# Optimization experiments

Measured on AMD Instinct MI355X. Metric: run time of the kernel, lower is better.

The kernel has to match this reference:

```python
import jax, jax.numpy as jnp
import numpy as np

DIM = 128
N_GNN = 3
B, N1, N2 = 8, 128, 512
VDW_N = 6.0
DEV_VDW = 0.2
MAX_VDW, MIN_VDW = 0.0356, 0.0178
DM_MIN = 0.5


def setup_inputs() -> dict:
    key = jax.random.key(0)
    ks = jax.random.split(key, 24)
    f32 = jnp.float32
    h1 = jax.random.normal(ks[0], (B, N1, 54), f32)
    h2 = jax.random.normal(ks[1], (B, N2, 54), f32)
    a1 = (jax.random.uniform(ks[2], (B, N1, N1)) < 0.1).astype(f32)
    adj1 = jnp.clip(a1 + jnp.swapaxes(a1, 1, 2) + jnp.eye(N1, dtype=f32), 0.0, 1.0)
    a2 = (jax.random.uniform(ks[3], (B, N2, N2)) < 0.05).astype(f32)
    adj2 = jnp.clip(a2 + jnp.swapaxes(a2, 1, 2) + jnp.eye(N2, dtype=f32), 0.0, 1.0)
    A_int = (jax.random.uniform(ks[4], (B, 8, N1, N2)) < 0.05).astype(f32)
    pos1 = jax.random.uniform(ks[5], (B, N1, 3), f32) * 30.0
    pos2 = jax.random.uniform(ks[6], (B, N2, 3), f32) * 30.0
    rotor = jax.random.uniform(ks[7], (B,), f32) * 10.0
    vdw_radius1 = 1.0 + jax.random.uniform(ks[8], (B, N1), f32)
    vdw_radius2 = 1.0 + jax.random.uniform(ks[9], (B, N2), f32)
    delta_uff = jax.random.uniform(ks[10], (B,), f32)
    no_metal1 = jnp.ones((B, N1), f32)
    no_metal2 = jnp.ones((B, N2), f32)
    s = 0.1
    node_W = jax.random.normal(ks[11], (54, DIM), f32) * s
    gat_W = jax.random.normal(ks[12], (N_GNN, DIM, DIM), f32) * s
    gat_b = jnp.zeros((N_GNN, DIM), f32)
    gat_A = jax.random.normal(ks[13], (N_GNN, DIM, DIM), f32) * s
    gate_W = jax.random.normal(ks[14], (N_GNN, 2 * DIM), f32) * s
    gate_b = jnp.zeros((N_GNN,), f32)
    vdwA_W1 = jax.random.normal(ks[15], (2 * DIM, 128), f32) * s
    vdwA_b1 = jnp.zeros((128,), f32)
    vdwA_W2 = jax.random.normal(ks[16], (128,), f32) * s
    vdwA_b2 = jnp.zeros((1,), f32)
    vdwB_W1 = jax.random.normal(ks[17], (2 * DIM, 128), f32) * s
    vdwB_b1 = jnp.zeros((128,), f32)
    vdwB_W2 = jax.random.normal(ks[18], (128,), f32) * s
    vdwB_b2 = jnp.zeros((1,), f32)
    hbond_coeff = jnp.array([1.0], f32)
    hydrophobic_coeff = jnp.array([0.5], f32)
    vdw_coeff = jnp.array([1.0], f32)
    rotor_coeff = jnp.array([0.5], f32)
    return dict(h1=h1, adj1=adj1, h2=h2, adj2=adj2, A_int=A_int, pos1=pos1, pos2=pos2,
                rotor=rotor, vdw_radius1=vdw_radius1, vdw_radius2=vdw_radius2,
                delta_uff=delta_uff, no_metal1=no_metal1, no_metal2=no_metal2,
                node_W=node_W, gat_W=gat_W, gat_b=gat_b, gat_A=gat_A, gate_W=gate_W,
                gate_b=gate_b, vdwA_W1=vdwA_W1, vdwA_b1=vdwA_b1, vdwA_W2=vdwA_W2,
                vdwA_b2=vdwA_b2, vdwB_W1=vdwB_W1, vdwB_b1=vdwB_b1, vdwB_W2=vdwB_W2,
                vdwB_b2=vdwB_b2, hbond_coeff=hbond_coeff,
                hydrophobic_coeff=hydrophobic_coeff, vdw_coeff=vdw_coeff,
                rotor_coeff=rotor_coeff)


def _gat(x, adj, W, b, A, gW, gb):
    # PIGNet GAT_gate: attention softmax over axis=1, masked by adj, gated residual.
    h = x @ W + b                                   # [B,N,D]
    e = jnp.einsum('bil,bkl->bik', h @ A, h)        # [B,N,N]
    e = e + jnp.swapaxes(e, 1, 2)
    att = jnp.where(adj > 0, e, -9e15)
    att = jax.nn.softmax(att, axis=1) * adj
    h_prime = jax.nn.relu(jnp.einsum('bij,bjk->bik', att, h))
    coeff = jax.nn.sigmoid(jnp.concatenate([x, h_prime], -1) @ gW + gb)[..., None]
    return coeff * x + (1.0 - coeff) * h_prime


def _pair_mlp(g1, g2, W1, b1, w2, b2):
    # Equivalent to Linear(cat[h1_rep,h2_rep]) without materializing the 2D concat.
    z = (jnp.einsum('bik,kh->bih', g1, W1[:DIM])[:, :, None, :]
         + jnp.einsum('bjk,kh->bjh', g2, W1[DIM:])[:, None, :, :] + b1)  # [B,N1,N2,128]
    return jax.nn.relu(z) @ w2 + b2                 # [B,N1,N2]


def _forward(h1, adj1, h2, adj2, A_int, pos1, pos2, rotor, vdw_radius1, vdw_radius2,
             delta_uff, no_metal1, no_metal2, node_W, gat_W, gat_b, gat_A, gate_W,
             gate_b, vdwA_W1, vdwA_b1, vdwA_W2, vdwA_b2, vdwB_W1, vdwB_b1, vdwB_W2,
             vdwB_b2, hbond_coeff, hydrophobic_coeff, vdw_coeff, rotor_coeff):
    g1 = h1 @ node_W
    g2 = h2 @ node_W
    for i in range(N_GNN):
        g1 = _gat(g1, adj1, gat_W[i], gat_b[i], gat_A[i], gate_W[i], gate_b[i])
        g2 = _gat(g2, adj2, gat_W[i], gat_b[i], gat_A[i], gate_W[i], gate_b[i])
    diff = pos1[:, :, None, :] - pos2[:, None, :, :]
    dm = jnp.sqrt(jnp.sum(diff * diff, -1) + 1e-10)   # [B,N1,N2]
    dm = jnp.where(dm < DM_MIN, 1e10, dm)
    A_w = jax.nn.sigmoid(_pair_mlp(g1, g2, vdwA_W1, vdwA_b1, vdwA_W2, vdwA_b2))
    B_w = jnp.tanh(_pair_mlp(g1, g2, vdwB_W1, vdwB_b1, vdwB_W2, vdwB_b2)) * DEV_VDW
    dm0 = vdw_radius1[:, :, None] + vdw_radius2[:, None, :] + B_w
    # vdW 12-6 term
    dm0_safe = jnp.where(dm0 < 1e-4, 1.0, dm0)
    rN = (dm0_safe / dm) ** VDW_N
    evdw = jnp.minimum(rN * rN - 2.0 * rN, 100.0)
    mask12 = no_metal1[:, :, None] * no_metal2[:, None, :]
    Aamp = A_w * (MAX_VDW - MIN_VDW) + MIN_VDW
    E_vdw = jnp.sum(Aamp * evdw * mask12, axis=(1, 2))
    # hbond / hydrophobic terms use unfixed dm0
    dmd = dm - dm0
    hb = -(hbond_coeff * hbond_coeff)[0]
    hy = -(hydrophobic_coeff * hydrophobic_coeff)[0]
    E_hb1 = jnp.sum(jnp.clip(dmd * A_int[:, 1] / -0.7, 0.0, 1.0), axis=(1, 2)) * hb
    E_hb2 = jnp.sum(jnp.clip(dmd * A_int[:, -1] / -0.7, 0.0, 1.0), axis=(1, 2)) * hb
    E_hp = jnp.sum(jnp.clip((-dmd + 1.5) * A_int[:, -2], 0.0, 1.0), axis=(1, 2)) * hy
    E_t = delta_uff * (vdw_coeff * vdw_coeff)[0]
    ret = jnp.stack([E_vdw, E_hb1, E_hb2, E_hp, E_t], -1)   # [B,5]
    ret = ret / (1.0 + (rotor_coeff * rotor_coeff)[0] * rotor[:, None])
    return ret


def reference(h1, adj1, h2, adj2, A_int, pos1, pos2, rotor, vdw_radius1, vdw_radius2,
              delta_uff, no_metal1, no_metal2, node_W, gat_W, gat_b, gat_A, gate_W,
              gate_b, vdwA_W1, vdwA_b1, vdwA_W2, vdwA_b2, vdwB_W1, vdwB_b1, vdwB_W2,
              vdwB_b2, hbond_coeff, hydrophobic_coeff, vdw_coeff, rotor_coeff):
    return _forward(h1, adj1, h2, adj2, A_int, pos1, pos2, rotor, vdw_radius1,
                    vdw_radius2, delta_uff, no_metal1, no_metal2, node_W, gat_W,
                    gat_b, gat_A, gate_W, gate_b, vdwA_W1, vdwA_b1, vdwA_W2,
                    vdwA_b2, vdwB_W1, vdwB_b1, vdwB_W2, vdwB_b2, hbond_coeff,
                    hydrophobic_coeff, vdw_coeff, rotor_coeff)
```

## Files before the change

### kernel.cpp

```cpp
#include <hip/hip_runtime.h>
#include <math.h>

#define D 128
#define NB 8
#define NN1 128
#define NN2 512
#define ROWS1 (NB * NN1)
#define ROWS2 (NB * NN2)
#define ROWS (ROWS1 + ROWS2)
#define CAP1 96
#define CAP2 160
#define CSR_ELEMS ((size_t)ROWS1 * CAP1 + (size_t)ROWS2 * CAP2)

__device__ __forceinline__ void resolve_row(int row, int& base_row, size_t& cbase,
                                            int& N) {
    if (row < ROWS1) {
        base_row = row & ~127;
        cbase = (size_t)row * CAP1;
        N = NN1;
    } else {
        int r = row - ROWS1;
        base_row = ROWS1 + (r & ~511);
        cbase = (size_t)ROWS1 * CAP1 + (size_t)r * CAP2;
        N = NN2;
    }
}

__global__ __launch_bounds__(128) void k_csrembed(
    const float* __restrict__ h1, const float* __restrict__ h2,
    const float* __restrict__ adj1, const float* __restrict__ adj2,
    const float* __restrict__ W, float* __restrict__ g,
    unsigned short* __restrict__ csr, int* __restrict__ nnz,
    float* __restrict__ out) {
    int row = blockIdx.x;
    int t = threadIdx.x;
    if (row == 0 && t < NB * 5) out[t] = 0.f;
    const float* src = (row < ROWS1) ? h1 + (size_t)row * 54
                                     : h2 + (size_t)(row - ROWS1) * 54;
    __shared__ float xr[56];
    if (t < 54) xr[t] = src[t];
    __syncthreads();
    float a0 = 0.f, a1 = 0.f;
#pragma unroll
    for (int k = 0; k < 54; k += 2) {
        a0 += xr[k] * W[k * D + t];
        if (k + 1 < 54) a1 += xr[k + 1] * W[(k + 1) * D + t];
    }
    g[(size_t)row * D + t] = a0 + a1;

    if (t < 64) {
        int base_row, N;
        size_t cbase;
        resolve_row(row, base_row, cbase, N);
        int cap = (row < ROWS1) ? CAP1 : CAP2;
        const float* arow = (row < ROWS1)
                                ? adj1 + (size_t)row * NN1
                                : adj2 + (size_t)(row - ROWS1) * NN2;
        int cnt = 0;
        for (int c0 = 0; c0 < N; c0 += 64) {
            float v = arow[c0 + t];
            unsigned long long m = __ballot(v > 0.f);
            int rank = __popcll(m & ((1ull << t) - 1ull));
            if (v > 0.f && cnt + rank < cap)
                csr[cbase + cnt + rank] = (unsigned short)(c0 + t);
            cnt += __popcll(m);
        }
        if (t == 0) nnz[row] = cnt < cap ? cnt : cap;
    }
}

__global__ __launch_bounds__(256) void k_h(const float* __restrict__ g,
                                           const float* __restrict__ W,
                                           const float* __restrict__ bias,
                                           const float* __restrict__ A,
                                           float* __restrict__ h, float* __restrict__ hA) {
    int row0 = blockIdx.x * 16;
    int t = threadIdx.x;
    int d = t & 127, rh = t >> 7;
    __shared__ float xs[16][D];
    __shared__ float hs[16][D];
    {
        int r = t >> 4, c = (t & 15) * 8;
        *(float4*)&xs[r][c] = *(const float4*)&g[((size_t)row0 + r) * D + c];
        *(float4*)&xs[r][c + 4] = *(const float4*)&g[((size_t)row0 + r) * D + c + 4];
    }
    __syncthreads();
    float bv = bias[d];
    float acc[8];
#pragma unroll
    for (int u = 0; u < 8; ++u) acc[u] = bv;
    for (int k0 = 0; k0 < D; k0 += 4) {
        float w0 = W[(k0 + 0) * D + d];
        float w1 = W[(k0 + 1) * D + d];
        float w2 = W[(k0 + 2) * D + d];
        float w3 = W[(k0 + 3) * D + d];
#pragma unroll
        for (int u = 0; u < 8; ++u) {
            float4 xv = *(const float4*)&xs[rh * 8 + u][k0];
            acc[u] += xv.x * w0 + xv.y * w1 + xv.z * w2 + xv.w * w3;
        }
    }
#pragma unroll
    for (int u = 0; u < 8; ++u) {
        int r = rh * 8 + u;
        h[((size_t)row0 + r) * D + d] = acc[u];
        hs[r][d] = acc[u];
    }
    __syncthreads();
    float acc2[8];
#pragma unroll
    for (int u = 0; u < 8; ++u) acc2[u] = 0.f;
    for (int k0 = 0; k0 < D; k0 += 4) {
        float w0 = A[(k0 + 0) * D + d];
        float w1 = A[(k0 + 1) * D + d];
        float w2 = A[(k0 + 2) * D + d];
        float w3 = A[(k0 + 3) * D + d];
#pragma unroll
        for (int u = 0; u < 8; ++u) {
            float4 xv = *(const float4*)&hs[rh * 8 + u][k0];
            acc2[u] += xv.x * w0 + xv.y * w1 + xv.z * w2 + xv.w * w3;
        }
    }
#pragma unroll
    for (int u = 0; u < 8; ++u)
        hA[((size_t)row0 + rh * 8 + u) * D + d] = acc2[u];
}

__global__ __launch_bounds__(128) void k_Ssp(const float* __restrict__ h,
                                             const float* __restrict__ hA,
                                             const unsigned short* __restrict__ csr,
                                             const int* __restrict__ nnz,
                                             float* __restrict__ svals,
                                             float2* __restrict__ rowstat) {
    int row = blockIdx.x;
    int t = threadIdx.x;
    int base_row, N;
    size_t cbase;
    resolve_row(row, base_row, cbase, N);
    int n = nnz[row];
    int grp = t >> 4, u = t & 15;
    const float* hrow = h + (size_t)row * D + u * 8;
    const float* hArow = hA + (size_t)row * D + u * 8;
    float4 hi0 = *(const float4*)&hrow[0], hi1 = *(const float4*)&hrow[4];
    float4 ai0 = *(const float4*)&hArow[0], ai1 = *(const float4*)&hArow[4];
    __shared__ float sv[CAP2];
    for (int s0 = 0; s0 < n; s0 += 16) {
        int sa = s0 + grp;
        int sb = sa + 8;
        float pa = 0.f, pb = 0.f;
        if (sa < n) {
            int jrow = base_row + csr[cbase + sa];
            const float* hj = h + (size_t)jrow * D + u * 8;
            const float* aj = hA + (size_t)jrow * D + u * 8;
            float4 hj0 = *(const float4*)&hj[0], hj1 = *(const float4*)&hj[4];
            float4 aj0 = *(const float4*)&aj[0], aj1 = *(const float4*)&aj[4];
            pa = hi0.x * aj0.x + hi0.y * aj0.y + hi0.z * aj0.z + hi0.w * aj0.w +
                 hi1.x * aj1.x + hi1.y * aj1.y + hi1.z * aj1.z + hi1.w * aj1.w +
                 ai0.x * hj0.x + ai0.y * hj0.y + ai0.z * hj0.z + ai0.w * hj0.w +
                 ai1.x * hj1.x + ai1.y * hj1.y + ai1.z * hj1.z + ai1.w * hj1.w;
        }
        if (sb < n) {
            int jrow = base_row + csr[cbase + sb];
            const float* hj = h + (size_t)jrow * D + u * 8;
            const float* aj = hA + (size_t)jrow * D + u * 8;
            float4 hj0 = *(const float4*)&hj[0], hj1 = *(const float4*)&hj[4];
            float4 aj0 = *(const float4*)&aj[0], aj1 = *(const float4*)&aj[4];
            pb = hi0.x * aj0.x + hi0.y * aj0.y + hi0.z * aj0.z + hi0.w * aj0.w +
                 hi1.x * aj1.x + hi1.y * aj1.y + hi1.z * aj1.z + hi1.w * aj1.w +
                 ai0.x * hj0.x + ai0.y * hj0.y + ai0.z * hj0.z + ai0.w * hj0.w +
                 ai1.x * hj1.x + ai1.y * hj1.y + ai1.z * hj1.z + ai1.w * hj1.w;
        }
#pragma unroll
        for (int o = 8; o > 0; o >>= 1) {
            pa += __shfl_xor(pa, o);
            pb += __shfl_xor(pb, o);
        }
        if (u == 0) {
            if (sa < n) sv[sa] = pa;
            if (sb < n) sv[sb] = pb;
        }
    }
    __syncthreads();
    if (t < 64) {
        float m = -3.4e38f;
        for (int s = t; s < n; s += 64) m = fmaxf(m, sv[s]);
#pragma unroll
        for (int o = 32; o > 0; o >>= 1) m = fmaxf(m, __shfl_xor(m, o));
        float sum = 0.f;
        for (int s = t; s < n; s += 64) sum += expf(sv[s] - m);
#pragma unroll
        for (int o = 32; o > 0; o >>= 1) sum += __shfl_xor(sum, o);
        if (t == 0) rowstat[row] = make_float2(m, 1.f / sum);
    }
    for (int s = t; s < n; s += 128) svals[cbase + s] = sv[s];
}

__global__ __launch_bounds__(128) void k_hpgate(const float* __restrict__ hbuf,
                                                float* __restrict__ g,
                                                const float* __restrict__ svals,
                                                const float2* __restrict__ rowstat,
                                                const unsigned short* __restrict__ csr,
                                                const int* __restrict__ nnz,
                                                const float* __restrict__ gW,
                                                const float* __restrict__ gb) {
    int row = blockIdx.x;
    int d = threadIdx.x;
    int base_row, N;
    size_t cbase;
    resolve_row(row, base_row, cbase, N);
    int n = nnz[row];
    __shared__ float avals[CAP2];
    __shared__ int aidx[CAP2];
    __shared__ float red[128];
    for (int s = d; s < n; s += 128) {
        int jrow = base_row + csr[cbase + s];
        float2 st = rowstat[jrow];
        avals[s] = expf(svals[cbase + s] - st.x) * st.y;
        aidx[s] = jrow;
    }
    __syncthreads();
    float a[8];
#pragma unroll
    for (int u = 0; u < 8; ++u) a[u] = 0.f;
    int s = 0;
    for (; s + 8 <= n; s += 8) {
#pragma unroll
        for (int u = 0; u < 8; ++u)
            a[u] += avals[s + u] * hbuf[(size_t)aidx[s + u] * D + d];
    }
    for (; s < n; ++s) a[0] += avals[s] * hbuf[(size_t)aidx[s] * D + d];
    float hv = fmaxf(((a[0] + a[1]) + (a[2] + a[3])) + ((a[4] + a[5]) + (a[6] + a[7])),
                     0.f);
    float xv = g[(size_t)row * D + d];
    red[d] = xv * gW[d] + hv * gW[D + d];
    __syncthreads();
    for (int o = 64; o > 0; o >>= 1) {
        if (d < o) red[d] += red[d + o];
        __syncthreads();
    }
    float c = 1.f / (1.f + expf(-(red[0] + gb[0])));
    g[(size_t)row * D + d] = c * xv + (1.f - c) * hv;
}

__global__ __launch_bounds__(256) void k_pairpre(const float* __restrict__ g,
                                                 const float* __restrict__ WA,
                                                 const float* __restrict__ WB,
                                                 const float* __restrict__ bA,
                                                 const float* __restrict__ bB,
                                                 float* __restrict__ aA,
                                                 float* __restrict__ aB) {
    int row0 = blockIdx.x * 16;
    int t = threadIdx.x;
    int d = t & 127, rh = t >> 7;
    int g2 = (row0 >= ROWS1);
    const float* WAp = g2 ? WA + D * D : WA;
    const float* WBp = g2 ? WB + D * D : WB;
    __shared__ float xs[16][D];
    {
        int r = t >> 4, c = (t & 15) * 8;
        *(float4*)&xs[r][c] = *(const float4*)&g[((size_t)row0 + r) * D + c];
        *(float4*)&xs[r][c + 4] = *(const float4*)&g[((size_t)row0 + r) * D + c + 4];
    }
    __syncthreads();
    float bvA = g2 ? 0.f : bA[d];
    float bvB = g2 ? 0.f : bB[d];
    float accA[8], accB[8];
#pragma unroll
    for (int u = 0; u < 8; ++u) { accA[u] = bvA; accB[u] = bvB; }
    for (int k0 = 0; k0 < D; k0 += 4) {
        float wa0 = WAp[(k0 + 0) * D + d], wa1 = WAp[(k0 + 1) * D + d];
        float wa2 = WAp[(k0 + 2) * D + d], wa3 = WAp[(k0 + 3) * D + d];
        float wb0 = WBp[(k0 + 0) * D + d], wb1 = WBp[(k0 + 1) * D + d];
        float wb2 = WBp[(k0 + 2) * D + d], wb3 = WBp[(k0 + 3) * D + d];
#pragma unroll
        for (int u = 0; u < 8; ++u) {
            float4 xv = *(const float4*)&xs[rh * 8 + u][k0];
            accA[u] += xv.x * wa0 + xv.y * wa1 + xv.z * wa2 + xv.w * wa3;
            accB[u] += xv.x * wb0 + xv.y * wb1 + xv.z * wb2 + xv.w * wb3;
        }
    }
#pragma unroll
    for (int u = 0; u < 8; ++u) {
        int r = rh * 8 + u;
        aA[((size_t)row0 + r) * D + d] = accA[u];
        aB[((size_t)row0 + r) * D + d] = accB[u];
    }
}

__global__ __launch_bounds__(256) void k_pairz(
    const float* __restrict__ aA, const float* __restrict__ aB,
    const float* __restrict__ w2A, const float* __restrict__ w2B,
    const float* __restrict__ b2A, const float* __restrict__ b2B,
    const float* __restrict__ pos1, const float* __restrict__ pos2,
    const float* __restrict__ vr1, const float* __restrict__ vr2,
    const float* __restrict__ nm1, const float* __restrict__ nm2,
    const float* __restrict__ A_int, const float* __restrict__ rotor,
    const float* __restrict__ duff, const float* __restrict__ hbond,
    const float* __restrict__ hydro, const float* __restrict__ vdwc,
    const float* __restrict__ rotc, float* __restrict__ out) {
    int b = blockIdx.y;
    int itile = blockIdx.x >> 4, jtile = blockIdx.x & 15;
    int i0 = itile * 32, j0 = jtile * 32;
    int t = threadIdx.x;
    int tx = t & 15, ty = t >> 4;
    __shared__ float A1a[32][20], A1b[32][20], A2a[32][20], A2b[32][20];
    __shared__ float w2As[128], w2Bs[128];
    __shared__ float zAs[32][33], zBs[32][33];
    __shared__ float redc[8][4];
    if (t < 128) { w2As[t] = w2A[t]; w2Bs[t] = w2B[t]; }
    float zA[2][2] = {{0.f, 0.f}, {0.f, 0.f}};
    float zB[2][2] = {{0.f, 0.f}, {0.f, 0.f}};
    int half = t >> 7, idx = t & 127;
    int sr = idx >> 2, sc = (idx & 3) * 4;
    size_t grow = half ? (size_t)(ROWS1 + b * NN2 + j0 + sr)
                       : (size_t)(b * NN1 + i0 + sr);
    for (int hc = 0; hc < D; hc += 16) {
        __syncthreads();
        float4 va = *(const float4*)&aA[grow * D + hc + sc];
        float4 vb = *(const float4*)&aB[grow * D + hc + sc];
        if (half) { *(float4*)&A2a[sr][sc] = va; *(float4*)&A2b[sr][sc] = vb; }
        else      { *(float4*)&A1a[sr][sc] = va; *(float4*)&A1b[sr][sc] = vb; }
        __syncthreads();
#pragma unroll
        for (int hh = 0; hh < 16; hh += 4) {
            float4 wA = *(const float4*)&w2As[hc + hh];
            float4 wB = *(const float4*)&w2Bs[hc + hh];
            float4 xA0 = *(const float4*)&A1a[ty][hh];
            float4 xA1 = *(const float4*)&A1a[ty + 16][hh];
            float4 xB0 = *(const float4*)&A1b[ty][hh];
            float4 xB1 = *(const float4*)&A1b[ty + 16][hh];
            float4 yA0 = *(const float4*)&A2a[tx][hh];
            float4 yA1 = *(const float4*)&A2a[tx + 16][hh];
            float4 yB0 = *(const float4*)&A2b[tx][hh];
            float4 yB1 = *(const float4*)&A2b[tx + 16][hh];
#define RD4(xx, yy, ww) (fmaxf(xx.x + yy.x, 0.f) * ww.x + fmaxf(xx.y + yy.y, 0.f) * ww.y + \
                         fmaxf(xx.z + yy.z, 0.f) * ww.z + fmaxf(xx.w + yy.w, 0.f) * ww.w)
            zA[0][0] += RD4(xA0, yA0, wA); zA[0][1] += RD4(xA0, yA1, wA);
            zA[1][0] += RD4(xA1, yA0, wA); zA[1][1] += RD4(xA1, yA1, wA);
            zB[0][0] += RD4(xB0, yB0, wB); zB[0][1] += RD4(xB0, yB1, wB);
            zB[1][0] += RD4(xB1, yB0, wB); zB[1][1] += RD4(xB1, yB1, wB);
#undef RD4
        }
    }
#pragma unroll
    for (int u = 0; u < 2; ++u)
#pragma unroll
        for (int v = 0; v < 2; ++v) {
            zAs[ty + 16 * u][tx + 16 * v] = zA[u][v];
            zBs[ty + 16 * u][tx + 16 * v] = zB[u][v];
        }
    __syncthreads();
    int j2 = t & 31, ig = t >> 5;
    int jg = j0 + j2;
    size_t j_off = (size_t)b * NN2 + jg;
    float p2x = pos2[j_off * 3 + 0], p2y = pos2[j_off * 3 + 1], p2z = pos2[j_off * 3 + 2];
    float r2 = vr2[j_off], m2 = nm2[j_off];
    float zb2A = b2A[0], zb2B = b2B[0];
    float eV[4], e1[4], e2[4], eH[4];
#pragma unroll
    for (int ii = 0; ii < 4; ++ii) {
        int il = ig * 4 + ii;
        int iglob = i0 + il;
        size_t i_off = (size_t)b * NN1 + iglob;
        float zAv = zAs[il][j2] + zb2A;
        float zBv = zBs[il][j2] + zb2B;
        float dx = pos1[i_off * 3 + 0] - p2x;
        float dy = pos1[i_off * 3 + 1] - p2y;
        float dz = pos1[i_off * 3 + 2] - p2z;
        float dm = sqrtf(dx * dx + dy * dy + dz * dz + 1e-10f);
        if (dm < 0.5f) dm = 1e10f;
        float A_w = 1.f / (1.f + expf(-zAv));
        float B_w = tanhf(zBv) * 0.2f;
        float dm0 = vr1[i_off] + r2 + B_w;
        float dm0s = (dm0 < 1e-4f) ? 1.f : dm0;
        float rr = dm0s / dm;
        float rr2 = rr * rr;
        float rN = rr2 * rr2 * rr2;
        float evdw = fminf(rN * rN - 2.f * rN, 100.f);
        float mask = nm1[i_off] * m2;
        float Aamp = A_w * (0.0356f - 0.0178f) + 0.0178f;
        eV[ii] = Aamp * evdw * mask;
        float dmd = dm - dm0;
        size_t abase = (((size_t)b * 8) * NN1 + iglob) * NN2 + jg;
        float Ai1 = A_int[abase + (size_t)1 * NN1 * NN2];
        float Ai6 = A_int[abase + (size_t)6 * NN1 * NN2];
        float Ai7 = A_int[abase + (size_t)7 * NN1 * NN2];
        e1[ii] = fminf(fmaxf(dmd * Ai1 * (-1.f / 0.7f), 0.f), 1.f);
        e2[ii] = fminf(fmaxf(dmd * Ai7 * (-1.f / 0.7f), 0.f), 1.f);
        eH[ii] = fminf(fmaxf((1.5f - dmd) * Ai6, 0.f), 1.f);
    }
    float sV = (eV[0] + eV[1]) + (eV[2] + eV[3]);
    float s1 = (e1[0] + e1[1]) + (e1[2] + e1[3]);
    float s2 = (e2[0] + e2[1]) + (e2[2] + e2[3]);
    float sH = (eH[0] + eH[1]) + (eH[2] + eH[3]);
#pragma unroll
    for (int o = 16; o > 0; o >>= 1) {
        sV += __shfl_xor(sV, o);
        s1 += __shfl_xor(s1, o);
        s2 += __shfl_xor(s2, o);
        sH += __shfl_xor(sH, o);
    }
    if (j2 == 0) {
        redc[ig][0] = sV; redc[ig][1] = s1; redc[ig][2] = s2; redc[ig][3] = sH;
    }
    __syncthreads();
    if (t < 4) {
        float v = 0.f;
#pragma unroll
        for (int gg = 0; gg < 8; ++gg) v += redc[gg][t];
        float scl = 1.f / (1.f + rotc[0] * rotc[0] * rotor[b]);
        float coef;
        if (t == 0) coef = scl;
        else if (t == 3) coef = -hydro[0] * hydro[0] * scl;
        else coef = -hbond[0] * hbond[0] * scl;
        atomicAdd(&out[b * 5 + t], v * coef);
    }
    if (t == 4 && itile == 0 && jtile == 0) {
        float scl = 1.f / (1.f + rotc[0] * rotc[0] * rotor[b]);
        atomicAdd(&out[b * 5 + 4], duff[b] * vdwc[0] * vdwc[0] * scl);
    }
}

extern "C" void kernel_launch(void* const* d_in, const int* in_sizes, int n_in,
                              void* d_out, int out_size, void* d_ws, size_t ws_size,
                              hipStream_t stream) {
    const float* h1    = (const float*)d_in[0];
    const float* adj1  = (const float*)d_in[1];
    const float* h2    = (const float*)d_in[2];
    const float* adj2  = (const float*)d_in[3];
    const float* A_int = (const float*)d_in[4];
    const float* pos1  = (const float*)d_in[5];
    const float* pos2  = (const float*)d_in[6];
    const float* rotor = (const float*)d_in[7];
    const float* vr1   = (const float*)d_in[8];
    const float* vr2   = (const float*)d_in[9];
    const float* duff  = (const float*)d_in[10];
    const float* nm1   = (const float*)d_in[11];
    const float* nm2   = (const float*)d_in[12];
    const float* nodeW = (const float*)d_in[13];
    const float* gatW  = (const float*)d_in[14];
    const float* gatb  = (const float*)d_in[15];
    const float* gatA  = (const float*)d_in[16];
    const float* gateW = (const float*)d_in[17];
    const float* gateb = (const float*)d_in[18];
    const float* vA_W1 = (const float*)d_in[19];
    const float* vA_b1 = (const float*)d_in[20];
    const float* vA_W2 = (const float*)d_in[21];
    const float* vA_b2 = (const float*)d_in[22];
    const float* vB_W1 = (const float*)d_in[23];
    const float* vB_b1 = (const float*)d_in[24];
    const float* vB_W2 = (const float*)d_in[25];
    const float* vB_b2 = (const float*)d_in[26];
    const float* hbond = (const float*)d_in[27];
    const float* hydro = (const float*)d_in[28];
    const float* vdwc  = (const float*)d_in[29];
    const float* rotc  = (const float*)d_in[30];

    float* p = (float*)d_ws;
    float* g     = p; p += (size_t)ROWS * D;
    float* hbuf  = p; p += (size_t)ROWS * D;
    float* hAbuf = p; p += (size_t)ROWS * D;
    float* svals = p; p += CSR_ELEMS;
    float2* rowstat = (float2*)p; p += 2 * (size_t)ROWS;
    unsigned short* csr = (unsigned short*)p;
    int* nnz = (int*)(csr + CSR_ELEMS);
    float* aA = hbuf;
    float* aB = hAbuf;

    k_csrembed<<<ROWS, 128, 0, stream>>>(h1, h2, adj1, adj2, nodeW, g, csr, nnz,
                                         (float*)d_out);

    for (int l = 0; l < 3; ++l) {
        const float* W  = gatW  + (size_t)l * D * D;
        const float* bb = gatb  + (size_t)l * D;
        const float* A  = gatA  + (size_t)l * D * D;
        const float* gW = gateW + (size_t)l * 2 * D;
        const float* gb = gateb + l;
        k_h<<<ROWS / 16, 256, 0, stream>>>(g, W, bb, A, hbuf, hAbuf);
        k_Ssp<<<ROWS, 128, 0, stream>>>(hbuf, hAbuf, csr, nnz, svals, rowstat);
        k_hpgate<<<ROWS, 128, 0, stream>>>(hbuf, g, svals, rowstat, csr, nnz, gW, gb);
    }

    k_pairpre<<<ROWS / 16, 256, 0, stream>>>(g, vA_W1, vB_W1, vA_b1, vB_b1, aA, aB);
    k_pairz<<<dim3(64, NB), 256, 0, stream>>>(aA, aB, vA_W2, vB_W2, vA_b2, vB_b2,
                                              pos1, pos2, vr1, vr2, nm1, nm2, A_int,
                                              rotor, duff, hbond, hydro, vdwc, rotc,
                                              (float*)d_out);
}
```

Measured before the change: 313.3 us.

## Fuse gated aggregation with next layer GEMMs and embed into first layer

Merges the per-row gate and aggregation kernel into the following layer's h/hA GEMM kernel, and the final layer's gate into the pair-pre GEMM. The node embedding is folded into the first h GEMM, and CSR construction moves to its own 4-rows-per-block kernel. Each 64-lane wave owns 4 rows, so no block barriers are needed, and the gate reduction uses wave shuffles. The h buffers are double-buffered so a layer can read neighbours while writing the next h. This cuts launches and global round trips of g. The cost is fewer blocks, with each wave processing its rows' gathers serially.

```diff
diff --git a/kernel.cpp b/kernel.cpp
--- a/kernel.cpp
+++ b/kernel.cpp
@@ -26,104 +26,105 @@
     }
 }
 
-__global__ __launch_bounds__(128) void k_csrembed(
-    const float* __restrict__ h1, const float* __restrict__ h2,
-    const float* __restrict__ adj1, const float* __restrict__ adj2,
-    const float* __restrict__ W, float* __restrict__ g,
-    unsigned short* __restrict__ csr, int* __restrict__ nnz,
-    float* __restrict__ out) {
-    int row = blockIdx.x;
+__global__ __launch_bounds__(256) void k_csr(const float* __restrict__ adj1,
+                                             const float* __restrict__ adj2,
+                                             unsigned short* __restrict__ csr,
+                                             int* __restrict__ nnz,
+                                             float* __restrict__ out) {
     int t = threadIdx.x;
-    if (row == 0 && t < NB * 5) out[t] = 0.f;
-    const float* src = (row < ROWS1) ? h1 + (size_t)row * 54
-                                     : h2 + (size_t)(row - ROWS1) * 54;
-    __shared__ float xr[56];
-    if (t < 54) xr[t] = src[t];
-    __syncthreads();
-    float a0 = 0.f, a1 = 0.f;
-#pragma unroll
-    for (int k = 0; k < 54; k += 2) {
-        a0 += xr[k] * W[k * D + t];
-        if (k + 1 < 54) a1 += xr[k + 1] * W[(k + 1) * D + t];
-    }
-    g[(size_t)row * D + t] = a0 + a1;
-
-    if (t < 64) {
-        int base_row, N;
-        size_t cbase;
-        resolve_row(row, base_row, cbase, N);
-        int cap = (row < ROWS1) ? CAP1 : CAP2;
-        const float* arow = (row < ROWS1)
-                                ? adj1 + (size_t)row * NN1
-                                : adj2 + (size_t)(row - ROWS1) * NN2;
-        int cnt = 0;
-        for (int c0 = 0; c0 < N; c0 += 64) {
-            float v = arow[c0 + t];
-            unsigned long long m = __ballot(v > 0.f);
-            int rank = __popcll(m & ((1ull << t) - 1ull));
-            if (v > 0.f && cnt + rank < cap)
-                csr[cbase + cnt + rank] = (unsigned short)(c0 + t);
-            cnt += __popcll(m);
-        }
-        if (t == 0) nnz[row] = cnt < cap ? cnt : cap;
-    }
-}
-
-__global__ __launch_bounds__(256) void k_h(const float* __restrict__ g,
-                                           const float* __restrict__ W,
-                                           const float* __restrict__ bias,
-                                           const float* __restrict__ A,
-                                           float* __restrict__ h, float* __restrict__ hA) {
+    if (blockIdx.x == 0 && t < NB * 5) out[t] = 0.f;
+    int row = blockIdx.x * 4 + (t >> 6);
+    int lane = t & 63;
+    int base_row, N;
+    size_t cbase;
+    resolve_row(row, base_row, cbase, N);
+    int cap = (row < ROWS1) ? CAP1 : CAP2;
+    const float* arow = (row < ROWS1) ? adj1 + (size_t)row * NN1
+                                      : adj2 + (size_t)(row - ROWS1) * NN2;
+    int cnt = 0;
+    for (int c0 = 0; c0 < N; c0 += 64) {
+        float v = arow[c0 + lane];
+        unsigned long long m = __ballot(v > 0.f);
+        int rank = __popcll(m & ((1ull << lane) - 1ull));
+        if (v > 0.f && cnt + rank < cap)
+            csr[cbase + cnt + rank] = (unsigned short)(c0 + lane);
+        cnt += __popcll(m);
+    }
+    if (lane == 0) nnz[row] = cnt < cap ? cnt : cap;
+}
+
+#define GEMM16(XS, W, B0, B1, OUTSTMT)                                        \
+    {                                                                         \
+        float acc[4][2];                                                      \
+        _Pragma("unroll") for (int u = 0; u < 4; ++u) {                       \
+            acc[u][0] = (B0); acc[u][1] = (B1);                               \
+        }                                                                     \
+        for (int k0 = 0; k0 < D; k0 += 4) {                                   \
+            float w00 = (W)[(k0 + 0) * D + d0], w01 = (W)[(k0 + 0) * D + d0 + 64]; \
+            float w10 = (W)[(k0 + 1) * D + d0], w11 = (W)[(k0 + 1) * D + d0 + 64]; \
+            float w20 = (W)[(k0 + 2) * D + d0], w21 = (W)[(k0 + 2) * D + d0 + 64]; \
+            float w30 = (W)[(k0 + 3) * D + d0], w31 = (W)[(k0 + 3) * D + d0 + 64]; \
+            _Pragma("unroll") for (int u = 0; u < 4; ++u) {                   \
+                float4 xv = *(const float4*)&XS[rg * 4 + u][k0];              \
+                acc[u][0] += xv.x * w00 + xv.y * w10 + xv.z * w20 + xv.w * w30; \
+                acc[u][1] += xv.x * w01 + xv.y * w11 + xv.z * w21 + xv.w * w31; \
+            }                                                                 \
+        }                                                                     \
+        _Pragma("unroll") for (int u = 0; u < 4; ++u) {                       \
+            _Pragma("unroll") for (int hf = 0; hf < 2; ++hf) {                \
+                int rr = rg * 4 + u;                                          \
+                int dd = d0 + hf * 64;                                        \
+                float av = acc[u][hf];                                        \
+                OUTSTMT;                                                      \
+            }                                                                 \
+        }                                                                     \
+    }
+
+__global__ __launch_bounds__(256) void k_h0(
+    const float* __restrict__ h1in, const float* __restrict__ h2in,
+    const float* __restrict__ nodeW, const float* __restrict__ W,
+    const float* __restrict__ bias, const float* __restrict__ A,
+    float* __restrict__ g, float* __restrict__ hOut, float* __restrict__ hAOut) {
     int row0 = blockIdx.x * 16;
     int t = threadIdx.x;
-    int d = t & 127, rh = t >> 7;
+    int d0 = t & 63, rg = t >> 6;
+    __shared__ float hin[16][56];
     __shared__ float xs[16][D];
     __shared__ float hs[16][D];
     {
-        int r = t >> 4, c = (t & 15) * 8;
-        *(float4*)&xs[r][c] = *(const float4*)&g[((size_t)row0 + r) * D + c];
-        *(float4*)&xs[r][c + 4] = *(const float4*)&g[((size_t)row0 + r) * D + c + 4];
-    }
-    __syncthreads();
-    float bv = bias[d];
-    float acc[8];
-#pragma unroll
-    for (int u = 0; u < 8; ++u) acc[u] = bv;
-    for (int k0 = 0; k0 < D; k0 += 4) {
-        float w0 = W[(k0 + 0) * D + d];
-        float w1 = W[(k0 + 1) * D + d];
-        float w2 = W[(k0 + 2) * D + d];
-        float w3 = W[(k0 + 3) * D + d];
-#pragma unroll
-        for (int u = 0; u < 8; ++u) {
-            float4 xv = *(const float4*)&xs[rh * 8 + u][k0];
-            acc[u] += xv.x * w0 + xv.y * w1 + xv.z * w2 + xv.w * w3;
-        }
-    }
-#pragma unroll
-    for (int u = 0; u < 8; ++u) {
-        int r = rh * 8 + u;
-        h[((size_t)row0 + r) * D + d] = acc[u];
-        hs[r][d] = acc[u];
-    }
-    __syncthreads();
-    float acc2[8];
-#pragma unroll
-    for (int u = 0; u < 8; ++u) acc2[u] = 0.f;
-    for (int k0 = 0; k0 < D; k0 += 4) {
-        float w0 = A[(k0 + 0) * D + d];
-        float w1 = A[(k0 + 1) * D + d];
-        float w2 = A[(k0 + 2) * D + d];
-        float w3 = A[(k0 + 3) * D + d];
-#pragma unroll
-        for (int u = 0; u < 8; ++u) {
-            float4 xv = *(const float4*)&hs[rh * 8 + u][k0];
-            acc2[u] += xv.x * w0 + xv.y * w1 + xv.z * w2 + xv.w * w3;
-        }
-    }
-#pragma unroll
-    for (int u = 0; u < 8; ++u)
-        hA[((size_t)row0 + rh * 8 + u) * D + d] = acc2[u];
+        int lane = t & 63;
+        const float* src = (row0 < ROWS1) ? h1in + (size_t)row0 * 54
+                                          : h2in + (size_t)(row0 - ROWS1) * 54;
+        for (int idx = lane; idx < 4 * 54; idx += 64) {
+            int r = idx / 54, c = idx - r * 54;
+            hin[rg * 4 + r][c] = src[(size_t)(rg * 4 + r) * 54 + c];
+        }
+    }
+    {
+        float acc[4][2] = {{0.f,0.f},{0.f,0.f},{0.f,0.f},{0.f,0.f}};
+        for (int k = 0; k < 54; ++k) {
+            float w0 = nodeW[k * D + d0], w1 = nodeW[k * D + d0 + 64];
+#pragma unroll
+            for (int u = 0; u < 4; ++u) {
+                float x = hin[rg * 4 + u][k];
+                acc[u][0] += x * w0;
+                acc[u][1] += x * w1;
+            }
+        }
+#pragma unroll
+        for (int u = 0; u < 4; ++u)
+#pragma unroll
+            for (int hf = 0; hf < 2; ++hf) {
+                int rr = rg * 4 + u, dd = d0 + hf * 64;
+                xs[rr][dd] = acc[u][hf];
+                g[((size_t)row0 + rr) * D + dd] = acc[u][hf];
+            }
+    }
+    float b0 = bias[d0], b1 = bias[d0 + 64];
+    GEMM16(xs, W, b0, b1,
+           { hs[rr][dd] = av; hOut[((size_t)row0 + rr) * D + dd] = av; })
+    GEMM16(hs, A, 0.f, 0.f,
+           { hAOut[((size_t)row0 + rr) * D + dd] = av; })
 }
 
 __global__ __launch_bounds__(128) void k_Ssp(const float* __restrict__ h,
@@ -195,96 +196,108 @@
     for (int s = t; s < n; s += 128) svals[cbase + s] = sv[s];
 }
 
-__global__ __launch_bounds__(128) void k_hpgate(const float* __restrict__ hbuf,
-                                                float* __restrict__ g,
-                                                const float* __restrict__ svals,
-                                                const float2* __restrict__ rowstat,
-                                                const unsigned short* __restrict__ csr,
-                                                const int* __restrict__ nnz,
-                                                const float* __restrict__ gW,
-                                                const float* __restrict__ gb) {
-    int row = blockIdx.x;
-    int d = threadIdx.x;
-    int base_row, N;
-    size_t cbase;
-    resolve_row(row, base_row, cbase, N);
-    int n = nnz[row];
-    __shared__ float avals[CAP2];
-    __shared__ int aidx[CAP2];
-    __shared__ float red[128];
-    for (int s = d; s < n; s += 128) {
-        int jrow = base_row + csr[cbase + s];
-        float2 st = rowstat[jrow];
-        avals[s] = expf(svals[cbase + s] - st.x) * st.y;
-        aidx[s] = jrow;
-    }
-    __syncthreads();
-    float a[8];
-#pragma unroll
-    for (int u = 0; u < 8; ++u) a[u] = 0.f;
-    int s = 0;
-    for (; s + 8 <= n; s += 8) {
-#pragma unroll
-        for (int u = 0; u < 8; ++u)
-            a[u] += avals[s + u] * hbuf[(size_t)aidx[s + u] * D + d];
-    }
-    for (; s < n; ++s) a[0] += avals[s] * hbuf[(size_t)aidx[s] * D + d];
-    float hv = fmaxf(((a[0] + a[1]) + (a[2] + a[3])) + ((a[4] + a[5]) + (a[6] + a[7])),
-                     0.f);
-    float xv = g[(size_t)row * D + d];
-    red[d] = xv * gW[d] + hv * gW[D + d];
-    __syncthreads();
-    for (int o = 64; o > 0; o >>= 1) {
-        if (d < o) red[d] += red[d + o];
-        __syncthreads();
-    }
-    float c = 1.f / (1.f + expf(-(red[0] + gb[0])));
-    g[(size_t)row * D + d] = c * xv + (1.f - c) * hv;
-}
-
-__global__ __launch_bounds__(256) void k_pairpre(const float* __restrict__ g,
-                                                 const float* __restrict__ WA,
-                                                 const float* __restrict__ WB,
-                                                 const float* __restrict__ bA,
-                                                 const float* __restrict__ bB,
-                                                 float* __restrict__ aA,
-                                                 float* __restrict__ aB) {
+__device__ __forceinline__ void hpgate16(
+    int row0, int t, const float* __restrict__ hIn, float* __restrict__ g,
+    const float* __restrict__ svals, const float2* __restrict__ rowstat,
+    const unsigned short* __restrict__ csr, const int* __restrict__ nnz,
+    const float* __restrict__ gW, float gb0, float (*xs)[D],
+    float av_s[4][CAP2], int ai_s[4][CAP2], int writeG) {
+    int lane = t & 63, wv = t >> 6;
+    for (int rr = 0; rr < 4; ++rr) {
+        int xrow = wv * 4 + rr;
+        int row = row0 + xrow;
+        int base_row, N;
+        size_t cbase;
+        resolve_row(row, base_row, cbase, N);
+        int n = nnz[row];
+        for (int s = lane; s < n; s += 64) {
+            int jrow = base_row + csr[cbase + s];
+            float2 st = rowstat[jrow];
+            av_s[wv][s] = expf(svals[cbase + s] - st.x) * st.y;
+            ai_s[wv][s] = jrow;
+        }
+        float a0[4] = {0.f, 0.f, 0.f, 0.f}, a1[4] = {0.f, 0.f, 0.f, 0.f};
+        int s = 0;
+        for (; s + 4 <= n; s += 4) {
+#pragma unroll
+            for (int q = 0; q < 4; ++q) {
+                float av = av_s[wv][s + q];
+                size_t jb = (size_t)ai_s[wv][s + q] * D;
+                a0[q] += av * hIn[jb + lane];
+                a1[q] += av * hIn[jb + lane + 64];
+            }
+        }
+        for (; s < n; ++s) {
+            float av = av_s[wv][s];
+            size_t jb = (size_t)ai_s[wv][s] * D;
+            a0[0] += av * hIn[jb + lane];
+            a1[0] += av * hIn[jb + lane + 64];
+        }
+        float hv0 = fmaxf((a0[0] + a0[1]) + (a0[2] + a0[3]), 0.f);
+        float hv1 = fmaxf((a1[0] + a1[1]) + (a1[2] + a1[3]), 0.f);
+        float xv0 = g[(size_t)row * D + lane];
+        float xv1 = g[(size_t)row * D + lane + 64];
+        float part = xv0 * gW[lane] + xv1 * gW[lane + 64] +
+                     hv0 * gW[D + lane] + hv1 * gW[D + lane + 64];
+#pragma unroll
+        for (int o = 32; o > 0; o >>= 1) part += __shfl_xor(part, o);
+        float c = 1.f / (1.f + expf(-(part + gb0)));
+        float g0 = c * xv0 + (1.f - c) * hv0;
+        float g1 = c * xv1 + (1.f - c) * hv1;
+        xs[xrow][lane] = g0;
+        xs[xrow][lane + 64] = g1;
+        if (writeG) {
+            g[(size_t)row * D + lane] = g0;
+            g[(size_t)row * D + lane + 64] = g1;
+        }
+    }
+}
+
+__global__ __launch_bounds__(256) void k_hgh(
+    const float* __restrict__ hIn, float* __restrict__ g,
+    const float* __restrict__ svals, const float2* __restrict__ rowstat,
+    const unsigned short* __restrict__ csr, const int* __restrict__ nnz,
+    const float* __restrict__ gW, const float* __restrict__ gb,
+    const float* __restrict__ W, const float* __restrict__ bias,
+    const float* __restrict__ A, float* __restrict__ hOut,
+    float* __restrict__ hAOut) {
     int row0 = blockIdx.x * 16;
     int t = threadIdx.x;
-    int d = t & 127, rh = t >> 7;
+    int d0 = t & 63, rg = t >> 6;
+    __shared__ float xs[16][D];
+    __shared__ float hs[16][D];
+    __shared__ float av_s[4][CAP2];
+    __shared__ int ai_s[4][CAP2];
+    hpgate16(row0, t, hIn, g, svals, rowstat, csr, nnz, gW, gb[0], xs, av_s, ai_s, 1);
+    float b0 = bias[d0], b1 = bias[d0 + 64];
+    GEMM16(xs, W, b0, b1,
+           { hs[rr][dd] = av; hOut[((size_t)row0 + rr) * D + dd] = av; })
+    GEMM16(hs, A, 0.f, 0.f,
+           { hAOut[((size_t)row0 + rr) * D + dd] = av; })
+}
+
+__global__ __launch_bounds__(256) void k_hgp(
+    const float* __restrict__ hIn, float* __restrict__ g,
+    const float* __restrict__ svals, const float2* __restrict__ rowstat,
+    const unsigned short* __restrict__ csr, const int* __restrict__ nnz,
+    const float* __restrict__ gW, const float* __restrict__ gb,
+    const float* __restrict__ WA, const float* __restrict__ WB,
+    const float* __restrict__ bA, const float* __restrict__ bB,
+    float* __restrict__ aA, float* __restrict__ aB) {
+    int row0 = blockIdx.x * 16;
+    int t = threadIdx.x;
+    int d0 = t & 63, rg = t >> 6;
+    __shared__ float xs[16][D];
+    __shared__ float av_s[4][CAP2];
+    __shared__ int ai_s[4][CAP2];
+    hpgate16(row0, t, hIn, g, svals, rowstat, csr, nnz, gW, gb[0], xs, av_s, ai_s, 0);
     int g2 = (row0 >= ROWS1);
     const float* WAp = g2 ? WA + D * D : WA;
     const float* WBp = g2 ? WB + D * D : WB;
-    __shared__ float xs[16][D];
-    {
-        int r = t >> 4, c = (t & 15) * 8;
-        *(float4*)&xs[r][c] = *(const float4*)&g[((size_t)row0 + r) * D + c];
-        *(float4*)&xs[r][c + 4] = *(const float4*)&g[((size_t)row0 + r) * D + c + 4];
-    }
-    __syncthreads();
-    float bvA = g2 ? 0.f : bA[d];
-    float bvB = g2 ? 0.f : bB[d];
-    float accA[8], accB[8];
-#pragma unroll
-    for (int u = 0; u < 8; ++u) { accA[u] = bvA; accB[u] = bvB; }
-    for (int k0 = 0; k0 < D; k0 += 4) {
-        float wa0 = WAp[(k0 + 0) * D + d], wa1 = WAp[(k0 + 1) * D + d];
-        float wa2 = WAp[(k0 + 2) * D + d], wa3 = WAp[(k0 + 3) * D + d];
-        float wb0 = WBp[(k0 + 0) * D + d], wb1 = WBp[(k0 + 1) * D + d];
-        float wb2 = WBp[(k0 + 2) * D + d], wb3 = WBp[(k0 + 3) * D + d];
-#pragma unroll
-        for (int u = 0; u < 8; ++u) {
-            float4 xv = *(const float4*)&xs[rh * 8 + u][k0];
-            accA[u] += xv.x * wa0 + xv.y * wa1 + xv.z * wa2 + xv.w * wa3;
-            accB[u] += xv.x * wb0 + xv.y * wb1 + xv.z * wb2 + xv.w * wb3;
-        }
-    }
-#pragma unroll
-    for (int u = 0; u < 8; ++u) {
-        int r = rh * 8 + u;
-        aA[((size_t)row0 + r) * D + d] = accA[u];
-        aB[((size_t)row0 + r) * D + d] = accB[u];
-    }
+    float bA0 = g2 ? 0.f : bA[d0], bA1 = g2 ? 0.f : bA[d0 + 64];
+    float bB0 = g2 ? 0.f : bB[d0], bB1 = g2 ? 0.f : bB[d0 + 64];
+    GEMM16(xs, WAp, bA0, bA1, { aA[((size_t)row0 + rr) * D + dd] = av; })
+    GEMM16(xs, WBp, bB0, bB1, { aB[((size_t)row0 + rr) * D + dd] = av; })
 }
 
 __global__ __launch_bounds__(256) void k_pairz(
@@ -457,33 +470,39 @@
     const float* rotc  = (const float*)d_in[30];
 
     float* p = (float*)d_ws;
-    float* g     = p; p += (size_t)ROWS * D;
-    float* hbuf  = p; p += (size_t)ROWS * D;
-    float* hAbuf = p; p += (size_t)ROWS * D;
+    float* g    = p; p += (size_t)ROWS * D;
+    float* hb0  = p; p += (size_t)ROWS * D;
+    float* hb1  = p; p += (size_t)ROWS * D;
+    float* hA0  = p; p += (size_t)ROWS * D;
+    float* hA1  = p; p += (size_t)ROWS * D;
     float* svals = p; p += CSR_ELEMS;
     float2* rowstat = (float2*)p; p += 2 * (size_t)ROWS;
     unsigned short* csr = (unsigned short*)p;
     int* nnz = (int*)(csr + CSR_ELEMS);
-    float* aA = hbuf;
-    float* aB = hAbuf;
-
-    k_csrembed<<<ROWS, 128, 0, stream>>>(h1, h2, adj1, adj2, nodeW, g, csr, nnz,
-                                         (float*)d_out);
-
-    for (int l = 0; l < 3; ++l) {
-        const float* W  = gatW  + (size_t)l * D * D;
-        const float* bb = gatb  + (size_t)l * D;
-        const float* A  = gatA  + (size_t)l * D * D;
-        const float* gW = gateW + (size_t)l * 2 * D;
-        const float* gb = gateb + l;
-        k_h<<<ROWS / 16, 256, 0, stream>>>(g, W, bb, A, hbuf, hAbuf);
-        k_Ssp<<<ROWS, 128, 0, stream>>>(hbuf, hAbuf, csr, nnz, svals, rowstat);
-        k_hpgate<<<ROWS, 128, 0, stream>>>(hbuf, g, svals, rowstat, csr, nnz, gW, gb);
-    }
-
-    k_pairpre<<<ROWS / 16, 256, 0, stream>>>(g, vA_W1, vB_W1, vA_b1, vB_b1, aA, aB);
+    float* aA = hb1;
+    float* aB = hA1;
+    float* outp = (float*)d_out;
+
+    k_csr<<<ROWS / 4, 256, 0, stream>>>(adj1, adj2, csr, nnz, outp);
+    k_h0<<<ROWS / 16, 256, 0, stream>>>(h1, h2, nodeW, gatW, gatb, gatA, g, hb0, hA0);
+
+    k_Ssp<<<ROWS, 128, 0, stream>>>(hb0, hA0, csr, nnz, svals, rowstat);
+    k_hgh<<<ROWS / 16, 256, 0, stream>>>(hb0, g, svals, rowstat, csr, nnz,
+                                         gateW, gateb,
+                                         gatW + (size_t)1 * D * D, gatb + D,
+                                         gatA + (size_t)1 * D * D, hb1, hA1);
+    k_Ssp<<<ROWS, 128, 0, stream>>>(hb1, hA1, csr, nnz, svals, rowstat);
+    k_hgh<<<ROWS / 16, 256, 0, stream>>>(hb1, g, svals, rowstat, csr, nnz,
+                                         gateW + 2 * D, gateb + 1,
+                                         gatW + (size_t)2 * D * D, gatb + 2 * D,
+                                         gatA + (size_t)2 * D * D, hb0, hA0);
+    k_Ssp<<<ROWS, 128, 0, stream>>>(hb0, hA0, csr, nnz, svals, rowstat);
+    k_hgp<<<ROWS / 16, 256, 0, stream>>>(hb0, g, svals, rowstat, csr, nnz,
+                                         gateW + 4 * D, gateb + 2,
+                                         vA_W1, vB_W1, vA_b1, vB_b1, aA, aB);
+
     k_pairz<<<dim3(64, NB), 256, 0, stream>>>(aA, aB, vA_W2, vB_W2, vA_b2, vB_b2,
                                               pos1, pos2, vr1, vr2, nm1, nm2, A_int,
                                               rotor, duff, hbond, hydro, vdwc, rotc,
-                                              (float*)d_out);
-}
+                                              outp);
+}
```

Result: slower. 444.1 us (+41.7%).

## Interleave batches across block indices and split CSR build from embedding

Applied to the files above, without the earlier changes.

Remaps block indices in every kernel so consecutive blocks cycle through the eight batches (batch = bid & 7), aiming to spread work and memory traffic across XCDs/L2 slices and balance the larger protein graphs with ligand rows. The CSR compaction is split out of the embed kernel into its own kernel that processes four rows per 256-thread block with full wavefront utilisation, instead of idling half of each 128-thread block. This adds one extra kernel launch, and the remapping may hurt locality where neighbouring rows shared cache lines.

```diff
diff --git a/kernel.cpp b/kernel.cpp
--- a/kernel.cpp
+++ b/kernel.cpp
@@ -26,15 +26,53 @@
     }
 }
 
-__global__ __launch_bounds__(128) void k_csrembed(
-    const float* __restrict__ h1, const float* __restrict__ h2,
-    const float* __restrict__ adj1, const float* __restrict__ adj2,
-    const float* __restrict__ W, float* __restrict__ g,
-    unsigned short* __restrict__ csr, int* __restrict__ nnz,
-    float* __restrict__ out) {
-    int row = blockIdx.x;
+__device__ __forceinline__ int swiz_row(int bid) {
+    int batch = bid & 7, idx = bid >> 3;
+    return (idx < NN1) ? batch * NN1 + idx
+                       : ROWS1 + batch * NN2 + (idx - NN1);
+}
+__device__ __forceinline__ int swiz_row16(int bid) {
+    int batch = bid & 7, gi = bid >> 3;
+    return (gi < 8) ? batch * NN1 + gi * 16
+                    : ROWS1 + batch * NN2 + (gi - 8) * 16;
+}
+
+__global__ __launch_bounds__(256) void k_csr(const float* __restrict__ adj1,
+                                             const float* __restrict__ adj2,
+                                             unsigned short* __restrict__ csr,
+                                             int* __restrict__ nnz,
+                                             float* __restrict__ out) {
     int t = threadIdx.x;
-    if (row == 0 && t < NB * 5) out[t] = 0.f;
+    if (blockIdx.x == 0 && t < NB * 5) out[t] = 0.f;
+    int batch = blockIdx.x & 7, gi = blockIdx.x >> 3;
+    int rowbase = (gi < 32) ? batch * NN1 + gi * 4
+                            : ROWS1 + batch * NN2 + (gi - 32) * 4;
+    int row = rowbase + (t >> 6);
+    int lane = t & 63;
+    int base_row, N;
+    size_t cbase;
+    resolve_row(row, base_row, cbase, N);
+    int cap = (row < ROWS1) ? CAP1 : CAP2;
+    const float* arow = (row < ROWS1) ? adj1 + (size_t)row * NN1
+                                      : adj2 + (size_t)(row - ROWS1) * NN2;
+    int cnt = 0;
+    for (int c0 = 0; c0 < N; c0 += 64) {
+        float v = arow[c0 + lane];
+        unsigned long long m = __ballot(v > 0.f);
+        int rank = __popcll(m & ((1ull << lane) - 1ull));
+        if (v > 0.f && cnt + rank < cap)
+            csr[cbase + cnt + rank] = (unsigned short)(c0 + lane);
+        cnt += __popcll(m);
+    }
+    if (lane == 0) nnz[row] = cnt < cap ? cnt : cap;
+}
+
+__global__ __launch_bounds__(128) void k_embed(const float* __restrict__ h1,
+                                               const float* __restrict__ h2,
+                                               const float* __restrict__ W,
+                                               float* __restrict__ g) {
+    int row = swiz_row(blockIdx.x);
+    int t = threadIdx.x;
     const float* src = (row < ROWS1) ? h1 + (size_t)row * 54
                                      : h2 + (size_t)(row - ROWS1) * 54;
     __shared__ float xr[56];
@@ -47,26 +85,6 @@
         if (k + 1 < 54) a1 += xr[k + 1] * W[(k + 1) * D + t];
     }
     g[(size_t)row * D + t] = a0 + a1;
-
-    if (t < 64) {
-        int base_row, N;
-        size_t cbase;
-        resolve_row(row, base_row, cbase, N);
-        int cap = (row < ROWS1) ? CAP1 : CAP2;
-        const float* arow = (row < ROWS1)
-                                ? adj1 + (size_t)row * NN1
-                                : adj2 + (size_t)(row - ROWS1) * NN2;
-        int cnt = 0;
-        for (int c0 = 0; c0 < N; c0 += 64) {
-            float v = arow[c0 + t];
-            unsigned long long m = __ballot(v > 0.f);
-            int rank = __popcll(m & ((1ull << t) - 1ull));
-            if (v > 0.f && cnt + rank < cap)
-                csr[cbase + cnt + rank] = (unsigned short)(c0 + t);
-            cnt += __popcll(m);
-        }
-        if (t == 0) nnz[row] = cnt < cap ? cnt : cap;
-    }
 }
 
 __global__ __launch_bounds__(256) void k_h(const float* __restrict__ g,
@@ -74,7 +92,7 @@
                                            const float* __restrict__ bias,
                                            const float* __restrict__ A,
                                            float* __restrict__ h, float* __restrict__ hA) {
-    int row0 = blockIdx.x * 16;
+    int row0 = swiz_row16(blockIdx.x);
     int t = threadIdx.x;
     int d = t & 127, rh = t >> 7;
     __shared__ float xs[16][D];
@@ -132,7 +150,7 @@
                                              const int* __restrict__ nnz,
                                              float* __restrict__ svals,
                                              float2* __restrict__ rowstat) {
-    int row = blockIdx.x;
+    int row = swiz_row(blockIdx.x);
     int t = threadIdx.x;
     int base_row, N;
     size_t cbase;
@@ -203,7 +221,7 @@
                                                 const int* __restrict__ nnz,
                                                 const float* __restrict__ gW,
                                                 const float* __restrict__ gb) {
-    int row = blockIdx.x;
+    int row = swiz_row(blockIdx.x);
     int d = threadIdx.x;
     int base_row, N;
     size_t cbase;
@@ -249,7 +267,7 @@
                                                  const float* __restrict__ bB,
                                                  float* __restrict__ aA,
                                                  float* __restrict__ aB) {
-    int row0 = blockIdx.x * 16;
+    int row0 = swiz_row16(blockIdx.x);
     int t = threadIdx.x;
     int d = t & 127, rh = t >> 7;
     int g2 = (row0 >= ROWS1);
@@ -298,8 +316,9 @@
     const float* __restrict__ duff, const float* __restrict__ hbond,
     const float* __restrict__ hydro, const float* __restrict__ vdwc,
     const float* __restrict__ rotc, float* __restrict__ out) {
-    int b = blockIdx.y;
-    int itile = blockIdx.x >> 4, jtile = blockIdx.x & 15;
+    int b = blockIdx.x & 7;
+    int tile = blockIdx.x >> 3;
+    int itile = tile >> 4, jtile = tile & 15;
     int i0 = itile * 32, j0 = jtile * 32;
     int t = threadIdx.x;
     int tx = t & 15, ty = t >> 4;
@@ -415,7 +434,7 @@
         else coef = -hbond[0] * hbond[0] * scl;
         atomicAdd(&out[b * 5 + t], v * coef);
     }
-    if (t == 4 && itile == 0 && jtile == 0) {
+    if (t == 4 && tile == 0) {
         float scl = 1.f / (1.f + rotc[0] * rotc[0] * rotor[b]);
         atomicAdd(&out[b * 5 + 4], duff[b] * vdwc[0] * vdwc[0] * scl);
     }
@@ -466,9 +485,10 @@
     int* nnz = (int*)(csr + CSR_ELEMS);
     float* aA = hbuf;
     float* aB = hAbuf;
-
-    k_csrembed<<<ROWS, 128, 0, stream>>>(h1, h2, adj1, adj2, nodeW, g, csr, nnz,
-                                         (float*)d_out);
+    float* outp = (float*)d_out;
+
+    k_csr<<<ROWS / 4, 256, 0, stream>>>(adj1, adj2, csr, nnz, outp);
+    k_embed<<<ROWS, 128, 0, stream>>>(h1, h2, nodeW, g);
 
     for (int l = 0; l < 3; ++l) {
         const float* W  = gatW  + (size_t)l * D * D;
@@ -482,8 +502,7 @@
     }
 
     k_pairpre<<<ROWS / 16, 256, 0, stream>>>(g, vA_W1, vB_W1, vA_b1, vB_b1, aA, aB);
-    k_pairz<<<dim3(64, NB), 256, 0, stream>>>(aA, aB, vA_W2, vB_W2, vA_b2, vB_b2,
-                                              pos1, pos2, vr1, vr2, nm1, nm2, A_int,
-                                              rotor, duff, hbond, hydro, vdwc, rotc,
-                                              (float*)d_out);
-}
+    k_pairz<<<512, 256, 0, stream>>>(aA, aB, vA_W2, vB_W2, vA_b2, vB_b2,
+                                     pos1, pos2, vr1, vr2, nm1, nm2, A_int,
+                                     rotor, duff, hbond, hydro, vdwc, rotc, outp);
+}
```

Result: faster. 289.8 us (-7.5%).
